# Kernel tuning notes

Hardware: AMD Instinct MI355X
Metric: run time of the kernel (lower is better)

The kernel has to match this reference:

```python
import jax, jax.numpy as jnp
import numpy as np

MINI_BLOCK = 4

def setup_inputs() -> dict:
    key = jax.random.key(0)
    k1, k2 = jax.random.split(key)
    B, IN, OUT = 4096, 4096, 4096
    gy, gx = OUT // MINI_BLOCK, IN // MINI_BLOCK
    x = jax.random.normal(k1, (B, IN), dtype=jnp.float32)
    eigens = jax.random.normal(k2, (gy, gx, MINI_BLOCK), dtype=jnp.float32)
    return {"x": x, "eigens": eigens}

def reference(x, eigens):
    # Block-circulant linear: out[b, y, :] = sum_x circconv(eigens[y, x], x_blk[b, x])
    # computed in the frequency domain. Original code used two-sided rfft +
    # complex_mult + irfft per (b, y, x) block and summed over x; since the FFT
    # and complex product are linear, we contract over x in frequency space
    # with an einsum instead of materializing the (B, gy, gx, block) tensor.
    gy, gx, blk = eigens.shape
    xb = x.reshape(-1, gx, blk)                      # (B, gx, blk)
    f_eig = jnp.fft.rfft(eigens, axis=-1)            # (gy, gx, blk//2+1) complex
    f_x = jnp.fft.rfft(xb, axis=-1)                  # (B, gx, blk//2+1)
    f_out = jnp.einsum('yxk,bxk->byk', f_eig, f_x)   # contract over gx
    out = jnp.fft.irfft(f_out, n=blk, axis=-1)       # (B, gy, blk)
    return out.reshape(-1, gy * blk)
```

## Files before the change

### kernel.cpp

```cpp
#include <hip/hip_runtime.h>


typedef __attribute__((ext_vector_type(8))) short bf16x8_t;
typedef __attribute__((ext_vector_type(4))) float f32x4_t;
typedef __attribute__((ext_vector_type(8))) unsigned short u16x8;

#define NDIM 4096
#define TILE 128
#define BK 32

__device__ __forceinline__ unsigned short f2bf(float f) {
    unsigned int u = __builtin_bit_cast(unsigned int, f);
    u += 0x7fffu + ((u >> 16) & 1u);
    return (unsigned short)(u >> 16);
}

__device__ __forceinline__ void async_copy16(const void* g, void* l) {
    __builtin_amdgcn_global_load_lds(
        (const __attribute__((address_space(1))) void*)g,
        (__attribute__((address_space(3))) void*)l,
        16, 0, 0);
}


__global__ __launch_bounds__(256) void pre_k(const float* __restrict__ x,
                                             const float* __restrict__ eig,
                                             unsigned short* __restrict__ xp,
                                             unsigned short* __restrict__ B) {
    if (blockIdx.x < 16384) {
        int gid = blockIdx.x * 256 + threadIdx.x;
        int b = gid >> 10, j = gid & 1023;
        float4 v = ((const float4*)x)[(size_t)b * 1024 + j];
        float r = v.x - v.z, m = v.w - v.y;
        unsigned short* dst = xp + (size_t)b * 5120 + j;
        dst[0]    = f2bf(v.x + v.y + v.z + v.w);
        dst[1024] = f2bf(r);
        dst[2048] = f2bf(m);
        dst[3072] = f2bf(r + m);
        dst[4096] = f2bf(v.x - v.y + v.z - v.w);
    } else {
        int gid = (blockIdx.x - 16384) * 256 + threadIdx.x;
        int y = gid >> 10, c = gid & 1023;
        float4 v = ((const float4*)eig)[(size_t)y * 1024 + c];
        float r = v.x - v.z, m = v.w - v.y;
        size_t p = (size_t)y * 1024 + c;
        B[p]            = f2bf(v.x + v.y + v.z + v.w);
        B[p + 1048576u] = f2bf(r);
        B[p + 2097152u] = f2bf(m - r);
        B[p + 3145728u] = f2bf(m + r);
        B[p + 4194304u] = f2bf(v.x - v.y + v.z - v.w);
    }
}

__global__ __launch_bounds__(256, 5) void gemm_k(
        const unsigned short* __restrict__ A,
        const unsigned short* __restrict__ B,
        float* __restrict__ C,
        float* __restrict__ K3) {
    __shared__ unsigned short lA[TILE * BK];
    __shared__ unsigned short lB[TILE * BK];

    const int aoffs[5] = {0, 3072, 1024, 2048, 4096};

    const int raw       = blockIdx.x;
    const int r_xcd     = raw & 7;
    const int local     = raw >> 3;
    const int nseg      = local & 7;
    const int pairLocal = local >> 3;
    const int p         = r_xcd * 20 + pairLocal;
    const int seg       = p >> 5;
    const int blkM      = p & 31;

    const int t    = threadIdx.x;
    const int lane = t & 63;
    const int w    = t >> 6;
    const int wm   = (w >> 1) * 64;
    const int wn   = (w & 1) * 64;
    const int lr   = lane & 15;
    const int quad = lane >> 4;

    const int e0 = t * 8;
    const int r0 = e0 >> 5;
    const int c0 = e0 & 31;

    const unsigned short* pa0 = A + (size_t)(blkM * TILE + r0) * 5120 + aoffs[seg] + c0;
    const unsigned short* pa1 = pa0 + (size_t)64 * 5120;
    const unsigned short* pb0 = B + (size_t)seg * 1048576 +
                                (size_t)(nseg * TILE + r0) * 1024 + c0;
    const unsigned short* pb1 = pb0 + (size_t)64 * 1024;

    unsigned short* dA0 = &lA[e0];
    unsigned short* dA1 = &lA[2048 + e0];
    unsigned short* dB0 = &lB[e0];
    unsigned short* dB1 = &lB[2048 + e0];

    const unsigned short* la0 = &lA[(wm + lr) * BK + quad * 8];
    const unsigned short* lb0 = &lB[(wn + lr) * BK + quad * 8];

    f32x4_t acc[4][4] = {};

    for (int k0 = 0; k0 < 1024; k0 += BK) {
        async_copy16(pa0 + k0, dA0);
        async_copy16(pa1 + k0, dA1);
        async_copy16(pb0 + k0, dB0);
        async_copy16(pb1 + k0, dB1);
        asm volatile("s_waitcnt vmcnt(0)" ::: "memory");
        __syncthreads();

        bf16x8_t af[4], bfr[4];
#pragma unroll
        for (int i = 0; i < 4; ++i)
            af[i] = *(const bf16x8_t*)(la0 + i * 16 * BK);
#pragma unroll
        for (int i = 0; i < 4; ++i)
            bfr[i] = *(const bf16x8_t*)(lb0 + i * 16 * BK);

#pragma unroll
        for (int mt = 0; mt < 4; ++mt)
#pragma unroll
            for (int nt = 0; nt < 4; ++nt)
                acc[mt][nt] = __builtin_amdgcn_mfma_f32_16x16x32_bf16(
                    af[mt], bfr[nt], acc[mt][nt], 0, 0, 0);

        __syncthreads();
    }

    float* dstbase;
    int    cstride, colbase;
    if (seg == 3) { dstbase = K3; cstride = 1024; colbase = nseg * TILE; }
    else {
        int regio = (seg < 3) ? seg : 3;
        dstbase = C; cstride = NDIM; colbase = regio * 1024 + nseg * TILE;
    }

    const int orow0 = blkM * TILE + wm + quad * 4;
    const int ocol0 = colbase + wn + lr;
#pragma unroll
    for (int mt = 0; mt < 4; ++mt) {
#pragma unroll
        for (int r = 0; r < 4; ++r) {
            float* dst = dstbase + (size_t)(orow0 + mt * 16 + r) * cstride + ocol0;
#pragma unroll
            for (int nt = 0; nt < 4; ++nt)
                dst[nt * 16] = acc[mt][nt][r];
        }
    }
}

__global__ __launch_bounds__(256) void post_k(float* __restrict__ O,
                                              const float* __restrict__ K3) {
    float* row = O + (size_t)blockIdx.x * NDIM;
    const float* k3row = K3 + (size_t)blockIdx.x * 1024;
    const int t = threadIdx.x;

    float4 v0 = *(const float4*)(row + 4 * t);
    float4 k1 = *(const float4*)(row + 1024 + 4 * t);
    float4 k2 = *(const float4*)(row + 2048 + 4 * t);
    float4 v2 = *(const float4*)(row + 3072 + 4 * t);
    float4 k3 = *(const float4*)(k3row + 4 * t);
    __syncthreads();

    const float* a0 = (const float*)&v0;
    const float* a1 = (const float*)&k1;
    const float* a2 = (const float*)&k2;
    const float* a3 = (const float*)&v2;
    const float* a4 = (const float*)&k3;
#pragma unroll
    for (int i = 0; i < 4; ++i) {
        float vr = a1[i] - a4[i];
        float vi = a1[i] + a2[i];
        float4 o;
        o.x = 0.25f * (a0[i] + 2.0f * vr + a3[i]);
        o.y = 0.25f * (a0[i] - 2.0f * vi - a3[i]);
        o.z = 0.25f * (a0[i] - 2.0f * vr + a3[i]);
        o.w = 0.25f * (a0[i] + 2.0f * vi - a3[i]);
        *(float4*)(row + 16 * t + 4 * i) = o;
    }
}


__global__ __launch_bounds__(256) void fwd_x_fb(const float* __restrict__ x,
                                                unsigned short* __restrict__ xp) {
    int gid = blockIdx.x * 256 + threadIdx.x;
    int b = gid >> 10, j = gid & 1023;
    float4 v = ((const float4*)x)[(size_t)b * 1024 + j];
    unsigned short* dst = xp + (size_t)b * NDIM + j;
    dst[0]    = f2bf(v.x + v.y + v.z + v.w);
    dst[1024] = f2bf(v.x - v.z);
    dst[2048] = f2bf(v.w - v.y);
    dst[3072] = f2bf(v.x - v.y + v.z - v.w);
}

__global__ __launch_bounds__(256) void build_b_fb(const float* __restrict__ eig,
                                                  unsigned short* __restrict__ B) {
    int gid = blockIdx.x * 256 + threadIdx.x;
    int y = gid >> 10, c = gid & 1023;
    float4 v = ((const float4*)eig)[(size_t)y * 1024 + c];
    float r = v.x - v.z, s = v.w - v.y;
    B[(size_t)y * 1024 + c] = f2bf(v.x + v.y + v.z + v.w);
    unsigned short* b1r = B + 1048576 + (size_t)y * 2048;
    b1r[c]        = f2bf(r);
    b1r[1024 + c] = f2bf(-s);
    unsigned short* b1i = B + 3145728 + (size_t)y * 2048;
    b1i[c]        = f2bf(s);
    b1i[1024 + c] = f2bf(r);
    B[5242880 + (size_t)y * 1024 + c] = f2bf(v.x - v.y + v.z - v.w);
}

__global__ __launch_bounds__(256, 2) void gemm_fb(
        const unsigned short* __restrict__ A,
        const unsigned short* __restrict__ B,
        float* __restrict__ C) {
    __shared__ unsigned short lA[TILE * BK];
    __shared__ unsigned short lB[TILE * BK];

    const int Ks[4]   = {1024, 2048, 2048, 1024};
    const int Aoff[4] = {0, 1024, 1024, 3072};
    const size_t Boff[4] = {0u, 1048576u, 3145728u, 5242880u};

    int lin = blockIdx.x;
    int seg, nseg, blkM;
    if (lin < 512) { seg = 1 + ((lin >> 3) & 1); nseg = lin & 7; blkM = lin >> 4; }
    else { int i = lin - 512; seg = ((i >> 3) & 1) * 3; nseg = i & 7; blkM = i >> 4; }

    const int K    = Ks[seg];
    const int aoff = Aoff[seg];
    const unsigned short* Bs = B + Boff[seg];

    const int t    = threadIdx.x;
    const int lane = t & 63;
    const int w    = t >> 6;
    const int wm   = (w >> 1) * 64;
    const int wn   = (w & 1) * 64;
    const int lr   = lane & 15;
    const int quad = lane >> 4;

    const int e0 = t * 8;
    const int r0 = e0 >> 5;
    const int c0 = e0 & 31;

    const unsigned short* pa0 = A + (size_t)(blkM * TILE + r0) * NDIM + aoff + c0;
    const unsigned short* pa1 = pa0 + (size_t)64 * NDIM;
    const unsigned short* pb0 = Bs + (size_t)(nseg * TILE + r0) * K + c0;
    const unsigned short* pb1 = pb0 + (size_t)64 * K;

    unsigned short* dA0 = &lA[e0];
    unsigned short* dA1 = &lA[2048 + e0];
    unsigned short* dB0 = &lB[e0];
    unsigned short* dB1 = &lB[2048 + e0];

    const unsigned short* la0 = &lA[(wm + lr) * BK + quad * 8];
    const unsigned short* lb0 = &lB[(wn + lr) * BK + quad * 8];

    f32x4_t acc[4][4] = {};

    for (int k0 = 0; k0 < K; k0 += BK) {
        async_copy16(pa0 + k0, dA0);
        async_copy16(pa1 + k0, dA1);
        async_copy16(pb0 + k0, dB0);
        async_copy16(pb1 + k0, dB1);
        asm volatile("s_waitcnt vmcnt(0)" ::: "memory");
        __syncthreads();

        bf16x8_t af[4], bfr[4];
#pragma unroll
        for (int i = 0; i < 4; ++i)
            af[i] = *(const bf16x8_t*)(la0 + i * 16 * BK);
#pragma unroll
        for (int i = 0; i < 4; ++i)
            bfr[i] = *(const bf16x8_t*)(lb0 + i * 16 * BK);

#pragma unroll
        for (int mt = 0; mt < 4; ++mt)
#pragma unroll
            for (int nt = 0; nt < 4; ++nt)
                acc[mt][nt] = __builtin_amdgcn_mfma_f32_16x16x32_bf16(
                    af[mt], bfr[nt], acc[mt][nt], 0, 0, 0);

        __syncthreads();
    }

    const int orow0 = blkM * TILE + wm + quad * 4;
    const int ocol0 = seg * 1024 + nseg * TILE + wn + lr;
#pragma unroll
    for (int mt = 0; mt < 4; ++mt) {
#pragma unroll
        for (int r = 0; r < 4; ++r) {
            float* dst = C + (size_t)(orow0 + mt * 16 + r) * NDIM + ocol0;
#pragma unroll
            for (int nt = 0; nt < 4; ++nt)
                dst[nt * 16] = acc[mt][nt][r];
        }
    }
}

__global__ __launch_bounds__(256) void post_fb(float* __restrict__ O) {
    float* row = O + (size_t)blockIdx.x * NDIM;
    const int t = threadIdx.x;
    float4 v0 = *(const float4*)(row + 4 * t);
    float4 vr = *(const float4*)(row + 1024 + 4 * t);
    float4 vi = *(const float4*)(row + 2048 + 4 * t);
    float4 v2 = *(const float4*)(row + 3072 + 4 * t);
    __syncthreads();
    const float* a0 = (const float*)&v0;
    const float* ar = (const float*)&vr;
    const float* ai = (const float*)&vi;
    const float* a2 = (const float*)&v2;
#pragma unroll
    for (int i = 0; i < 4; ++i) {
        float4 o;
        o.x = 0.25f * (a0[i] + 2.0f * ar[i] + a2[i]);
        o.y = 0.25f * (a0[i] - 2.0f * ai[i] - a2[i]);
        o.z = 0.25f * (a0[i] - 2.0f * ar[i] + a2[i]);
        o.w = 0.25f * (a0[i] + 2.0f * ai[i] - a2[i]);
        *(float4*)(row + 16 * t + 4 * i) = o;
    }
}


extern "C" void kernel_launch(void* const* d_in, const int* in_sizes, int n_in,
                              void* d_out, int out_size, void* d_ws, size_t ws_size,
                              hipStream_t stream) {
    const float* x   = (const float*)d_in[0];
    const float* eig = (const float*)d_in[1];
    float* out = (float*)d_out;

    const size_t NEED = (size_t)66 * 1024 * 1024;

    if (ws_size >= NEED) {
        unsigned short* Xp = (unsigned short*)d_ws;
        unsigned short* Bp = (unsigned short*)((char*)d_ws + 41943040u);
        float*          K3 = (float*)((char*)d_ws + 52428800u);

        pre_k<<<16384 + 4096, 256, 0, stream>>>(x, eig, Xp, Bp);
        gemm_k<<<1280, 256, 0, stream>>>(Xp, Bp, out, K3);
        post_k<<<NDIM, 256, 0, stream>>>(out, K3);
    } else {
        unsigned short* Xp = (unsigned short*)d_ws;
        unsigned short* Bp = Xp + (size_t)NDIM * NDIM;

        fwd_x_fb<<<(NDIM * 1024) / 256, 256, 0, stream>>>(x, Xp);
        build_b_fb<<<(1024 * 1024) / 256, 256, 0, stream>>>(eig, Bp);
        gemm_fb<<<dim3(1024, 1), 256, 0, stream>>>(Xp, Bp, out);
        post_fb<<<NDIM, 256, 0, stream>>>(out);
    }
}
```

Before: 213.5 us.

## Fuse frequency-bin GEMMs and post-processing into one double-buffered GEMM kernel

After: 188.3 us. 11.8% less time.

```diff
diff --git a/kernel.cpp b/kernel.cpp
--- a/kernel.cpp
+++ b/kernel.cpp
@@ -3,7 +3,6 @@
 
 typedef __attribute__((ext_vector_type(8))) short bf16x8_t;
 typedef __attribute__((ext_vector_type(4))) float f32x4_t;
-typedef __attribute__((ext_vector_type(8))) unsigned short u16x8;
 
 #define NDIM 4096
 #define TILE 128
@@ -27,154 +26,172 @@
                                              const float* __restrict__ eig,
                                              unsigned short* __restrict__ xp,
                                              unsigned short* __restrict__ B) {
-    if (blockIdx.x < 16384) {
-        int gid = blockIdx.x * 256 + threadIdx.x;
-        int b = gid >> 10, j = gid & 1023;
-        float4 v = ((const float4*)x)[(size_t)b * 1024 + j];
-        float r = v.x - v.z, m = v.w - v.y;
-        unsigned short* dst = xp + (size_t)b * 5120 + j;
-        dst[0]    = f2bf(v.x + v.y + v.z + v.w);
-        dst[1024] = f2bf(r);
-        dst[2048] = f2bf(m);
-        dst[3072] = f2bf(r + m);
-        dst[4096] = f2bf(v.x - v.y + v.z - v.w);
+    const int t = threadIdx.x;
+    if (blockIdx.x < 4096) {
+        int gid = blockIdx.x * 256 + t;
+        int b = gid >> 8, j0 = (gid & 255) << 2;
+        const float4* src = (const float4*)x + ((size_t)b << 10) + j0;
+        unsigned short S[4], R[4], Mi[4], Z[4], T[4];
+#pragma unroll
+        for (int q = 0; q < 4; ++q) {
+            float4 v = src[q];
+            float r = v.x - v.z, m = v.w - v.y;
+            S[q]  = f2bf(r + m);
+            R[q]  = f2bf(r);
+            Mi[q] = f2bf(m);
+            Z[q]  = f2bf(v.x + v.y + v.z + v.w);
+            T[q]  = f2bf(v.x - v.y + v.z - v.w);
+        }
+        unsigned short* dst = xp + (size_t)b * 5120 + j0;
+        *(ushort4*)(dst)        = *(const ushort4*)S;
+        *(ushort4*)(dst + 1024) = *(const ushort4*)R;
+        *(ushort4*)(dst + 2048) = *(const ushort4*)Mi;
+        *(ushort4*)(dst + 3072) = *(const ushort4*)Z;
+        *(ushort4*)(dst + 4096) = *(const ushort4*)T;
     } else {
-        int gid = (blockIdx.x - 16384) * 256 + threadIdx.x;
-        int y = gid >> 10, c = gid & 1023;
-        float4 v = ((const float4*)eig)[(size_t)y * 1024 + c];
-        float r = v.x - v.z, m = v.w - v.y;
-        size_t p = (size_t)y * 1024 + c;
-        B[p]            = f2bf(v.x + v.y + v.z + v.w);
-        B[p + 1048576u] = f2bf(r);
-        B[p + 2097152u] = f2bf(m - r);
-        B[p + 3145728u] = f2bf(m + r);
-        B[p + 4194304u] = f2bf(v.x - v.y + v.z - v.w);
-    }
-}
-
-__global__ __launch_bounds__(256, 5) void gemm_k(
+        int gid = (blockIdx.x - 4096) * 256 + t;
+        int y = gid >> 8, c0 = (gid & 255) << 2;
+        const float4* src = (const float4*)eig + ((size_t)y << 10) + c0;
+        unsigned short P0[4], P1[4], P2[4], P3[4], P4[4];
+#pragma unroll
+        for (int q = 0; q < 4; ++q) {
+            float4 v = src[q];
+            float r = v.x - v.z, m = v.w - v.y;
+            P0[q] = f2bf(r);
+            P1[q] = f2bf(m - r);
+            P2[q] = f2bf(-(m + r));
+            P3[q] = f2bf(v.x + v.y + v.z + v.w);
+            P4[q] = f2bf(v.x - v.y + v.z - v.w);
+        }
+        unsigned short* dst = B + (size_t)y * 5120 + c0;
+        *(ushort4*)(dst)        = *(const ushort4*)P0;
+        *(ushort4*)(dst + 1024) = *(const ushort4*)P1;
+        *(ushort4*)(dst + 2048) = *(const ushort4*)P2;
+        *(ushort4*)(dst + 3072) = *(const ushort4*)P3;
+        *(ushort4*)(dst + 4096) = *(const ushort4*)P4;
+    }
+}
+
+__global__ __launch_bounds__(512, 2) void gemm_f(
         const unsigned short* __restrict__ A,
         const unsigned short* __restrict__ B,
-        float* __restrict__ C,
-        float* __restrict__ K3) {
-    __shared__ unsigned short lA[TILE * BK];
-    __shared__ unsigned short lB[TILE * BK];
-
-    const int aoffs[5] = {0, 3072, 1024, 2048, 4096};
-
-    const int raw       = blockIdx.x;
-    const int r_xcd     = raw & 7;
-    const int local     = raw >> 3;
-    const int nseg      = local & 7;
-    const int pairLocal = local >> 3;
-    const int p         = r_xcd * 20 + pairLocal;
-    const int seg       = p >> 5;
-    const int blkM      = p & 31;
+        float* __restrict__ C) {
+    __shared__ unsigned short sm[2][16384];
+
+    const int raw    = blockIdx.x;
+    const int xcd    = raw & 7;
+    const int idx    = raw >> 3;
+    const int rowBlk = xcd * 4 + (idx >> 3);
+    const int colBlk = idx & 7;
 
     const int t    = threadIdx.x;
     const int lane = t & 63;
     const int w    = t >> 6;
-    const int wm   = (w >> 1) * 64;
-    const int wn   = (w & 1) * 64;
+    const int wm   = (w >> 2) * 64;
+    const int wn   = (w & 3) * 32;
     const int lr   = lane & 15;
     const int quad = lane >> 4;
-
-    const int e0 = t * 8;
-    const int r0 = e0 >> 5;
-    const int c0 = e0 & 31;
-
-    const unsigned short* pa0 = A + (size_t)(blkM * TILE + r0) * 5120 + aoffs[seg] + c0;
+    const int xr   = lr & 7;
+
+    const int srow = t >> 3;
+    const int scol = ((t & 7) ^ ((t >> 3) & 7)) << 3;
+    const unsigned short* pa0 = A + (size_t)(rowBlk * 128 + srow) * 5120 + scol;
     const unsigned short* pa1 = pa0 + (size_t)64 * 5120;
-    const unsigned short* pb0 = B + (size_t)seg * 1048576 +
-                                (size_t)(nseg * TILE + r0) * 1024 + c0;
-    const unsigned short* pb1 = pb0 + (size_t)64 * 1024;
-
-    unsigned short* dA0 = &lA[e0];
-    unsigned short* dA1 = &lA[2048 + e0];
-    unsigned short* dB0 = &lB[e0];
-    unsigned short* dB1 = &lB[2048 + e0];
-
-    const unsigned short* la0 = &lA[(wm + lr) * BK + quad * 8];
-    const unsigned short* lb0 = &lB[(wn + lr) * BK + quad * 8];
-
-    f32x4_t acc[4][4] = {};
-
-    for (int k0 = 0; k0 < 1024; k0 += BK) {
-        async_copy16(pa0 + k0, dA0);
-        async_copy16(pa1 + k0, dA1);
-        async_copy16(pb0 + k0, dB0);
-        async_copy16(pb1 + k0, dB1);
-        asm volatile("s_waitcnt vmcnt(0)" ::: "memory");
-        __syncthreads();
-
-        bf16x8_t af[4], bfr[4];
-#pragma unroll
-        for (int i = 0; i < 4; ++i)
-            af[i] = *(const bf16x8_t*)(la0 + i * 16 * BK);
-#pragma unroll
-        for (int i = 0; i < 4; ++i)
-            bfr[i] = *(const bf16x8_t*)(lb0 + i * 16 * BK);
-
-#pragma unroll
-        for (int mt = 0; mt < 4; ++mt)
-#pragma unroll
-            for (int nt = 0; nt < 4; ++nt)
-                acc[mt][nt] = __builtin_amdgcn_mfma_f32_16x16x32_bf16(
-                    af[mt], bfr[nt], acc[mt][nt], 0, 0, 0);
-
-        __syncthreads();
-    }
-
-    float* dstbase;
-    int    cstride, colbase;
-    if (seg == 3) { dstbase = K3; cstride = 1024; colbase = nseg * TILE; }
-    else {
-        int regio = (seg < 3) ? seg : 3;
-        dstbase = C; cstride = NDIM; colbase = regio * 1024 + nseg * TILE;
-    }
-
-    const int orow0 = blkM * TILE + wm + quad * 4;
-    const int ocol0 = colbase + wn + lr;
+    const unsigned short* pb0 = B + (size_t)(colBlk * 128 + srow) * 5120 + scol;
+    const unsigned short* pb1 = pb0 + (size_t)64 * 5120;
+
+    char* smb  = (char*)&sm[0][0];
+    char* dstT = smb + (size_t)t * 16;
+
+    int koff = 0;
+    int cur  = 0;
+
+    f32x4_t aK1[4][2] = {};
+    f32x4_t aOi[4][2];
+    f32x4_t aO0[4][2] = {};
+    f32x4_t aO2[4][2] = {};
+
+#define STAGE_F(BUF)                                           \
+    {                                                          \
+        char* d = dstT + (BUF) * 32768;                        \
+        async_copy16(pa0 + koff, d);                           \
+        async_copy16(pa1 + koff, d + 8192);                    \
+        async_copy16(pb0 + koff, d + 16384);                   \
+        async_copy16(pb1 + koff, d + 24576);                   \
+        koff += 64;                                            \
+    }
+
+#define COMPUTE_F(BUF, ACC)                                                   \
+    {                                                                         \
+        const char* ab = smb + (BUF) * 32768 + (wm + lr) * 128;               \
+        const char* bb = smb + (BUF) * 32768 + 16384 + (wn + lr) * 128;       \
+        _Pragma("unroll")                                                     \
+        for (int kk = 0; kk < 2; ++kk) {                                      \
+            const int sw = ((((kk << 2) | quad)) ^ xr) << 4;                  \
+            bf16x8_t af[4], bfv[2];                                           \
+            _Pragma("unroll")                                                 \
+            for (int i = 0; i < 4; ++i)                                       \
+                af[i] = *(const bf16x8_t*)(ab + i * 2048 + sw);               \
+            _Pragma("unroll")                                                 \
+            for (int j = 0; j < 2; ++j)                                       \
+                bfv[j] = *(const bf16x8_t*)(bb + j * 2048 + sw);              \
+            _Pragma("unroll")                                                 \
+            for (int mt = 0; mt < 4; ++mt)                                    \
+                _Pragma("unroll")                                             \
+                for (int nt = 0; nt < 2; ++nt)                                \
+                    ACC[mt][nt] = __builtin_amdgcn_mfma_f32_16x16x32_bf16(    \
+                        af[mt], bfv[nt], ACC[mt][nt], 0, 0, 0);               \
+        }                                                                     \
+    }
+
+#define PHASE_F(ACC, ISLAST)                                   \
+    _Pragma("unroll 2")                                        \
+    for (int s2 = 0; s2 < 16; ++s2) {                          \
+        if (!(ISLAST) || s2 < 15) STAGE_F(cur ^ 1);            \
+        COMPUTE_F(cur, ACC);                                   \
+        asm volatile("s_waitcnt vmcnt(0)" ::: "memory");       \
+        __syncthreads();                                       \
+        cur ^= 1;                                              \
+    }
+
+    STAGE_F(0);
+    asm volatile("s_waitcnt vmcnt(0)" ::: "memory");
+    __syncthreads();
+
+    PHASE_F(aK1, 0)
+#pragma unroll
+    for (int mt = 0; mt < 4; ++mt)
+#pragma unroll
+        for (int nt = 0; nt < 2; ++nt) aOi[mt][nt] = aK1[mt][nt];
+    PHASE_F(aOi, 0)
+    PHASE_F(aK1, 0)
+    PHASE_F(aO0, 0)
+    PHASE_F(aO2, 1)
+
+#undef PHASE_F
+#undef COMPUTE_F
+#undef STAGE_F
+
+    const int orow0 = rowBlk * 128 + wm + quad * 4;
+    const int yc0   = colBlk * 128 + wn + lr;
 #pragma unroll
     for (int mt = 0; mt < 4; ++mt) {
 #pragma unroll
         for (int r = 0; r < 4; ++r) {
-            float* dst = dstbase + (size_t)(orow0 + mt * 16 + r) * cstride + ocol0;
-#pragma unroll
-            for (int nt = 0; nt < 4; ++nt)
-                dst[nt * 16] = acc[mt][nt][r];
+            float* dst = C + (size_t)(orow0 + mt * 16 + r) * NDIM;
+#pragma unroll
+            for (int nt = 0; nt < 2; ++nt) {
+                int yc = yc0 + nt * 16;
+                float O0 = aO0[mt][nt][r], Or = aK1[mt][nt][r];
+                float Oi = aOi[mt][nt][r], O2 = aO2[mt][nt][r];
+                float4 o;
+                o.x = 0.25f * (O0 + 2.0f * Or + O2);
+                o.y = 0.25f * (O0 - 2.0f * Oi - O2);
+                o.z = 0.25f * (O0 - 2.0f * Or + O2);
+                o.w = 0.25f * (O0 + 2.0f * Oi - O2);
+                *(float4*)(dst + 4 * yc) = o;
+            }
         }
-    }
-}
-
-__global__ __launch_bounds__(256) void post_k(float* __restrict__ O,
-                                              const float* __restrict__ K3) {
-    float* row = O + (size_t)blockIdx.x * NDIM;
-    const float* k3row = K3 + (size_t)blockIdx.x * 1024;
-    const int t = threadIdx.x;
-
-    float4 v0 = *(const float4*)(row + 4 * t);
-    float4 k1 = *(const float4*)(row + 1024 + 4 * t);
-    float4 k2 = *(const float4*)(row + 2048 + 4 * t);
-    float4 v2 = *(const float4*)(row + 3072 + 4 * t);
-    float4 k3 = *(const float4*)(k3row + 4 * t);
-    __syncthreads();
-
-    const float* a0 = (const float*)&v0;
-    const float* a1 = (const float*)&k1;
-    const float* a2 = (const float*)&k2;
-    const float* a3 = (const float*)&v2;
-    const float* a4 = (const float*)&k3;
-#pragma unroll
-    for (int i = 0; i < 4; ++i) {
-        float vr = a1[i] - a4[i];
-        float vi = a1[i] + a2[i];
-        float4 o;
-        o.x = 0.25f * (a0[i] + 2.0f * vr + a3[i]);
-        o.y = 0.25f * (a0[i] - 2.0f * vi - a3[i]);
-        o.z = 0.25f * (a0[i] - 2.0f * vr + a3[i]);
-        o.w = 0.25f * (a0[i] + 2.0f * vi - a3[i]);
-        *(float4*)(row + 16 * t + 4 * i) = o;
     }
 }
 
@@ -325,16 +342,14 @@
     const float* eig = (const float*)d_in[1];
     float* out = (float*)d_out;
 
-    const size_t NEED = (size_t)66 * 1024 * 1024;
+    const size_t NEED = (size_t)50 * 1024 * 1024;
 
     if (ws_size >= NEED) {
         unsigned short* Xp = (unsigned short*)d_ws;
         unsigned short* Bp = (unsigned short*)((char*)d_ws + 41943040u);
-        float*          K3 = (float*)((char*)d_ws + 52428800u);
-
-        pre_k<<<16384 + 4096, 256, 0, stream>>>(x, eig, Xp, Bp);
-        gemm_k<<<1280, 256, 0, stream>>>(Xp, Bp, out, K3);
-        post_k<<<NDIM, 256, 0, stream>>>(out, K3);
+
+        pre_k<<<5120, 256, 0, stream>>>(x, eig, Xp, Bp);
+        gemm_f<<<256, 512, 0, stream>>>(Xp, Bp, out);
     } else {
         unsigned short* Xp = (unsigned short*)d_ws;
         unsigned short* Bp = Xp + (size_t)NDIM * NDIM;
```
